# Kernel optimization log

Measured on AMD Instinct MI355X. Metric: run time of the kernel, lower is better.

The kernel has to match this reference:

```python
import jax, jax.numpy as jnp
import numpy as np

N_NODES = 100000
N_EDGES = 1600000
IN_C, HID_C, OUT_C = 128, 128, 64


def setup_inputs() -> dict:
    key = jax.random.key(0)
    k1, k2, k3, k4 = jax.random.split(key, 4)
    x = jax.random.normal(k1, (N_NODES, IN_C), dtype=jnp.float32)
    edge_index = jax.random.randint(k2, (2, N_EDGES), 0, N_NODES, dtype=jnp.int32)
    # Glorot-style init scale for the linear weights (matches PyG GCNConv default)
    W1 = jax.random.normal(k3, (IN_C, HID_C), dtype=jnp.float32) * (1.0 / np.sqrt(IN_C))
    b1 = jnp.zeros((HID_C,), dtype=jnp.float32)
    W2 = jax.random.normal(k4, (HID_C, OUT_C), dtype=jnp.float32) * (1.0 / np.sqrt(HID_C))
    b2 = jnp.zeros((OUT_C,), dtype=jnp.float32)
    return {"x": x, "edge_index": edge_index, "W1": W1, "b1": b1, "W2": W2, "b2": b2}


def _gcn_norm(edge_index, num_nodes):
    """Add self-loops and compute symmetric normalization deg^-1/2[src]*deg^-1/2[dst]."""
    src, dst = edge_index[0], edge_index[1]
    loop = jnp.arange(num_nodes, dtype=src.dtype)
    src_f = jnp.concatenate([src, loop])
    dst_f = jnp.concatenate([dst, loop])
    ones = jnp.ones_like(dst_f, dtype=jnp.float32)
    deg = jax.ops.segment_sum(ones, dst_f, num_segments=num_nodes)  # in-degree incl. self-loop
    deg_inv_sqrt = jnp.where(deg > 0, jax.lax.rsqrt(deg), 0.0)
    norm = deg_inv_sqrt[src_f] * deg_inv_sqrt[dst_f]  # [E+N]
    return src_f, dst_f, norm


def _gcn_conv(x, W, b, src_f, dst_f, norm, num_nodes):
    h = x @ W                              # [N, C_out] linear transform first
    msg = h[src_f] * norm[:, None]         # gather + scale, [E+N, C_out]
    agg = jax.ops.segment_sum(msg, dst_f, num_segments=num_nodes)  # scatter-add
    return agg + b


def reference(x, edge_index, W1, b1, W2, b2):
    n = x.shape[0]
    src_f, dst_f, norm = _gcn_norm(edge_index, n)
    h = jax.nn.relu(_gcn_conv(x, W1, b1, src_f, dst_f, norm, n))
    out = _gcn_conv(h, W2, b2, src_f, dst_f, norm, n)
    return out
```

## Files before the change

kernel.cpp:

```cpp
#include <hip/hip_runtime.h>


constexpr int BLK = 256;
constexpr int PCAP = 2560;
constexpr int CHUNK = 2048;
constexpr int NBMAX = 800;


__global__ __launch_bounds__(256)
void count_kernel(const int* __restrict__ dst, unsigned short* __restrict__ cnt,
                  int e, int nbuck) {
    __shared__ int hist[NBMAX];
    const int t = threadIdx.x;
    const int base = blockIdx.x * CHUNK;
    const int cend = min(CHUNK, e - base);

    for (int i = t; i < nbuck; i += 256) hist[i] = 0;
    __syncthreads();
    for (int i = t; i < cend; i += 256) atomicAdd(&hist[dst[base + i] >> 7], 1);
    __syncthreads();
    unsigned short* o = cnt + (size_t)blockIdx.x * nbuck;
    for (int i = t; i < nbuck; i += 256) o[i] = (unsigned short)hist[i];
}


__global__ __launch_bounds__(256)
void scan_bins_kernel(unsigned short* __restrict__ cnt, int* __restrict__ totals,
                      int nbuck, int nblk) {
    __shared__ int wsum[256];
    const int j = blockIdx.x;
    const int t = threadIdx.x;
    const int b0 = t * 4;
    int v[4];
    int s = 0;
#pragma unroll
    for (int q = 0; q < 4; ++q) {
        const int B = b0 + q;
        v[q] = (B < nblk) ? (int)cnt[(size_t)B * nbuck + j] : 0;
        s += v[q];
    }
    wsum[t] = s;
    __syncthreads();
    for (int off = 1; off < 256; off <<= 1) {
        int u = (t >= off) ? wsum[t - off] : 0;
        __syncthreads();
        wsum[t] += u;
        __syncthreads();
    }
    int run = (t > 0) ? wsum[t - 1] : 0;
#pragma unroll
    for (int q = 0; q < 4; ++q) {
        const int B = b0 + q;
        if (B < nblk) {
            cnt[(size_t)B * nbuck + j] = (unsigned short)min(run, PCAP);
            run += v[q];
        }
    }
    if (t == 255) totals[j] = run;
}


__global__ __launch_bounds__(256)
void place_kernel(const int* __restrict__ src, const int* __restrict__ dst,
                  const unsigned short* __restrict__ cnt, unsigned* __restrict__ ebuf,
                  int e, int nbuck) {
    __shared__ unsigned stage[CHUNK];
    __shared__ unsigned short keys[CHUNK];
    __shared__ int hist[NBMAX];
    __shared__ int excl[NBMAX];
    __shared__ int gbase[NBMAX];
    __shared__ int wsum[256];

    const int t = threadIdx.x;
    const int base = blockIdx.x * CHUNK;
    const int cend = min(CHUNK, e - base);

    for (int i = t; i < nbuck; i += 256) hist[i] = 0;
    __syncthreads();

    int dreg[8];
#pragma unroll
    for (int q = 0; q < 8; ++q) {
        const int i = t + q * 256;
        dreg[q] = (i < cend) ? dst[base + i] : -1;
        if (i < cend) atomicAdd(&hist[dreg[q] >> 7], 1);
    }
    __syncthreads();

    const int b0 = t * 4;
    int s0 = 0, s1 = 0, s2 = 0, s3 = 0;
    if (b0 < nbuck)     s0 = hist[b0];
    if (b0 + 1 < nbuck) s1 = hist[b0 + 1];
    if (b0 + 2 < nbuck) s2 = hist[b0 + 2];
    if (b0 + 3 < nbuck) s3 = hist[b0 + 3];
    wsum[t] = s0 + s1 + s2 + s3;
    __syncthreads();
    for (int off = 1; off < 256; off <<= 1) {
        int u = (t >= off) ? wsum[t - off] : 0;
        __syncthreads();
        wsum[t] += u;
        __syncthreads();
    }
    int run = (t > 0) ? wsum[t - 1] : 0;
    if (b0 < nbuck)     { excl[b0]     = run; hist[b0]     = run; run += s0; }
    if (b0 + 1 < nbuck) { excl[b0 + 1] = run; hist[b0 + 1] = run; run += s1; }
    if (b0 + 2 < nbuck) { excl[b0 + 2] = run; hist[b0 + 2] = run; run += s2; }
    if (b0 + 3 < nbuck) { excl[b0 + 3] = run; hist[b0 + 3] = run; run += s3; }
    {
        const unsigned short* cb = cnt + (size_t)blockIdx.x * nbuck;
        for (int i = t; i < nbuck; i += 256) gbase[i] = (int)cb[i];
    }
    __syncthreads();

#pragma unroll
    for (int q = 0; q < 8; ++q) {
        const int i = t + q * 256;
        if (i < cend) {
            const int s = src[base + i], d = dreg[q];
            const int bb = d >> 7;
            const int p = atomicAdd(&hist[bb], 1);
            stage[p] = ((unsigned)s << 7) | (unsigned)(d & 127);
            keys[p] = (unsigned short)bb;
        }
    }
    __syncthreads();

    for (int i = t; i < cend; i += 256) {
        const int bb = keys[i];
        const int p = gbase[bb] + (i - excl[bb]);
        if (p < PCAP) ebuf[(size_t)bb * PCAP + p] = stage[i];
    }
}


__global__ __launch_bounds__(256)
void build_kernel(const unsigned* __restrict__ ebuf, const int* __restrict__ totals,
                  float* __restrict__ dis, int2* __restrict__ rp,
                  int* __restrict__ esrc, int n) {
    __shared__ int packed[PCAP];
    __shared__ unsigned short rank[PCAP];
    __shared__ int hist[128];
    __shared__ int excl[128];
    __shared__ int start[128];

    const int b = blockIdx.x, t = threadIdx.x;
    const int base = b << 7;
    const int nloc = min(128, n - base);
    const int tot = min(totals[b], PCAP);

    if (t < 128) hist[t] = 0;
    __syncthreads();

    const unsigned* eb = ebuf + (size_t)b * PCAP;
    for (int i = t; i < tot; i += 256) {
        int v = (int)eb[i];
        packed[i] = v;
        rank[i] = (unsigned short)atomicAdd(&hist[v & 127], 1);
    }
    __syncthreads();

    if (t < 128) excl[t] = hist[t];
    __syncthreads();
    for (int off = 1; off < 128; off <<= 1) {
        int v = (t >= off && t < 128) ? excl[t - off] : 0;
        __syncthreads();
        if (t < 128) excl[t] += v;
        __syncthreads();
    }

    if (t < 128) {
        int deg = hist[t];
        int st = excl[t] - deg;
        start[t] = st;
        if (t < nloc) {
            dis[base + t] = rsqrtf((float)(deg + 1));
            int gs = b * PCAP + st;
            rp[base + t] = make_int2(gs, gs + deg);
        }
    }
    __syncthreads();

    int* eo = esrc + b * PCAP;
    for (int i = t; i < tot; i += 256) {
        int v = packed[i];
        eo[start[v & 127] + rank[i]] = v >> 7;
    }
}


__device__ __forceinline__ unsigned short f2bf(float f) {
    unsigned u = __float_as_uint(f);
    u += 0x7fffu + ((u >> 16) & 1u);
    return (unsigned short)(u >> 16);
}
__device__ __forceinline__ float bflo(unsigned u) { return __uint_as_float(u << 16); }
__device__ __forceinline__ float bfhi(unsigned u) { return __uint_as_float(u & 0xffff0000u); }
__device__ __forceinline__ unsigned pk2(short a, short b) {
    return (unsigned)(unsigned short)a | ((unsigned)(unsigned short)b << 16);
}

__device__ __forceinline__ void split2(float v, short& hi, short& lo) {
    unsigned short h = f2bf(v);
    float hf = __uint_as_float(((unsigned)h) << 16);
    hi = (short)h;
    lo = (short)f2bf(v - hf);
}

typedef __attribute__((ext_vector_type(8))) short bf16x8;
typedef __attribute__((ext_vector_type(4))) float f32x4;
#define MFMA_B16(a, b, c) __builtin_amdgcn_mfma_f32_16x16x32_bf16(a, b, c, 0, 0, 0)

__device__ __forceinline__ void split8(const float4& a, const float4& b, bf16x8& h, bf16x8& l) {
    short hh, ll;
    split2(a.x, hh, ll); h[0] = hh; l[0] = ll;
    split2(a.y, hh, ll); h[1] = hh; l[1] = ll;
    split2(a.z, hh, ll); h[2] = hh; l[2] = ll;
    split2(a.w, hh, ll); h[3] = hh; l[3] = ll;
    split2(b.x, hh, ll); h[4] = hh; l[4] = ll;
    split2(b.y, hh, ll); h[5] = hh; l[5] = ll;
    split2(b.z, hh, ll); h[6] = hh; l[6] = ll;
    split2(b.w, hh, ll); h[7] = hh; l[7] = ll;
}


__global__ void prep_b_kernel(const float* __restrict__ W1, const float* __restrict__ W2,
                              unsigned short* __restrict__ B1h, unsigned short* __restrict__ B1l,
                              unsigned short* __restrict__ B2h, unsigned short* __restrict__ B2l) {
    const int c = blockIdx.x;
    const int k = threadIdx.x;
    short h, l;
    if (c < 128) {
        split2(W1[(size_t)k * 128 + c], h, l);
        B1h[c * 128 + k] = (unsigned short)h;
        B1l[c * 128 + k] = (unsigned short)l;
    } else {
        const int c2 = c - 128;
        split2(W2[(size_t)k * 64 + c2], h, l);
        B2h[c2 * 128 + k] = (unsigned short)h;
        B2l[c2 * 128 + k] = (unsigned short)l;
    }
}


constexpr int BAS = 72;

__global__ __launch_bounds__(256, 4)
void gemm_mfma(const float* __restrict__ Af,
               const unsigned short* __restrict__ Bh, const unsigned short* __restrict__ Bl,
               const float* __restrict__ dis, unsigned* __restrict__ Cb, int nrows) {
    constexpr int COLS = 128;
    constexpr int CT = COLS / 16;
    constexpr int BE = COLS * BAS;
    constexpr int CSC = COLS + 8;
    constexpr int SMEM = (2 * BE * 2 > 128 * CSC * 2) ? 2 * BE * 2 : 128 * CSC * 2;

    __shared__ __align__(16) char smem[SMEM];
    short* sBh = (short*)smem;
    short* sBl = sBh + BE;

    const int t = threadIdx.x;
    const int rowbase = blockIdx.x * 128;
    const int wave = t >> 6;
    const int lane = t & 63;
    const int quad = lane >> 4;
    const int l16 = lane & 15;

    const int gr0 = rowbase + wave * 32 + l16;
    const int gr1 = gr0 + 16;

    f32x4 acc[2][CT];
#pragma unroll
    for (int rt = 0; rt < 2; ++rt)
#pragma unroll
        for (int ct = 0; ct < CT; ++ct) {
            f32x4 z = {0.f, 0.f, 0.f, 0.f};
            acc[rt][ct] = z;
        }

    for (int half = 0; half < 2; ++half) {
        {
            constexpr int NV = COLS * 8;
            uint4* dh = (uint4*)sBh;
            uint4* dl = (uint4*)sBl;
            const uint4* gh = (const uint4*)Bh;
            const uint4* gl = (const uint4*)Bl;
            for (int idx = t; idx < NV; idx += 256) {
                int c = idx >> 3, kq = idx & 7;
                int gidx = c * 16 + half * 8 + kq;
                int didx = c * 9 + kq;
                dh[didx] = gh[gidx];
                dl[didx] = gl[gidx];
            }
        }
        __syncthreads();

#pragma unroll
        for (int kc = 0; kc < 2; ++kc) {
            const int ko = kc * 32 + quad * 8;
            bf16x8 ah0, al0, ah1, al1;
            float4 va = {0.f, 0.f, 0.f, 0.f}, vb = va, vc = va, vd = va;
            if (gr0 < nrows) {
                const float4* ap = (const float4*)(Af + (size_t)gr0 * 128 + half * 64 + ko);
                va = ap[0]; vb = ap[1];
            }
            if (gr1 < nrows) {
                const float4* ap = (const float4*)(Af + (size_t)gr1 * 128 + half * 64 + ko);
                vc = ap[0]; vd = ap[1];
            }
            split8(va, vb, ah0, al0);
            split8(vc, vd, ah1, al1);
#pragma unroll
            for (int ct = 0; ct < CT; ++ct) {
                const int bo = (ct * 16 + l16) * BAS + ko;
                bf16x8 bh = *(const bf16x8*)&sBh[bo];
                bf16x8 bl = *(const bf16x8*)&sBl[bo];
                acc[0][ct] = MFMA_B16(ah0, bh, acc[0][ct]);
                acc[1][ct] = MFMA_B16(ah1, bh, acc[1][ct]);
                acc[0][ct] = MFMA_B16(al0, bh, acc[0][ct]);
                acc[1][ct] = MFMA_B16(al1, bh, acc[1][ct]);
                acc[0][ct] = MFMA_B16(ah0, bl, acc[0][ct]);
                acc[1][ct] = MFMA_B16(ah1, bl, acc[1][ct]);
            }
        }
        __syncthreads();
    }

    short* Cs = (short*)smem;
    float sv[2][4];
#pragma unroll
    for (int rt = 0; rt < 2; ++rt)
#pragma unroll
        for (int r = 0; r < 4; ++r) {
            int rr = rowbase + wave * 32 + rt * 16 + quad * 4 + r;
            sv[rt][r] = (rr < nrows) ? dis[rr] : 0.f;
        }
#pragma unroll
    for (int rt = 0; rt < 2; ++rt)
#pragma unroll
        for (int ct = 0; ct < CT; ++ct) {
            const int rb = wave * 32 + rt * 16 + quad * 4;
            const int c = ct * 16 + l16;
#pragma unroll
            for (int r = 0; r < 4; ++r)
                Cs[(rb + r) * CSC + c] = (short)f2bf(sv[rt][r] * acc[rt][ct][r]);
        }
    __syncthreads();

    {
        const int row = t >> 1, hf = t & 1;
        const int gr = rowbase + row;
        if (gr < nrows) {
            const uint4* cr = (const uint4*)&Cs[row * CSC + hf * (COLS / 2)];
            uint4* dstp = (uint4*)Cb + (size_t)gr * (COLS / 8) + hf * (COLS / 16);
#pragma unroll
            for (int i = 0; i < COLS / 16; ++i) dstp[i] = cr[i];
        }
    }
}


#define ACC8(v)                                           \
    acc[0] += bflo(v.x); acc[1] += bfhi(v.x);             \
    acc[2] += bflo(v.y); acc[3] += bfhi(v.y);             \
    acc[4] += bflo(v.z); acc[5] += bfhi(v.z);             \
    acc[6] += bflo(v.w); acc[7] += bfhi(v.w);

__global__ __launch_bounds__(512)
void gather_gemm_kernel(const int2* __restrict__ rp, const int* __restrict__ esrc,
                        const float* __restrict__ dis, const unsigned* __restrict__ hs,
                        const float* __restrict__ bias,
                        const unsigned short* __restrict__ B2h,
                        const unsigned short* __restrict__ B2l,
                        unsigned* __restrict__ h2b, int n) {
    constexpr int ASTR = 136;
    constexpr int CSTR = 72;
    __shared__ __align__(16) short sAh[32 * ASTR];
    __shared__ __align__(16) short sAl[32 * ASTR];

    const int t = threadIdx.x;
    const int base = blockIdx.x * 32;

    {
        const int nl = t >> 4;
        const int lc = t & 15;
        const int node = base + nl;

        if (node < n) {
            const uint4* h4 = (const uint4*)hs;
            const int2 se = rp[node];
            float acc[8];
            {
                uint4 v = h4[(size_t)node * 16 + lc];
                acc[0] = bflo(v.x); acc[1] = bfhi(v.x);
                acc[2] = bflo(v.y); acc[3] = bfhi(v.y);
                acc[4] = bflo(v.z); acc[5] = bfhi(v.z);
                acc[6] = bflo(v.w); acc[7] = bfhi(v.w);
            }
            int k = se.x;
            const int end = se.y;
            for (; k + 3 < end; k += 4) {
                int s0 = esrc[k], s1 = esrc[k + 1], s2 = esrc[k + 2], s3 = esrc[k + 3];
                uint4 v0 = h4[(size_t)s0 * 16 + lc];
                uint4 v1 = h4[(size_t)s1 * 16 + lc];
                uint4 v2 = h4[(size_t)s2 * 16 + lc];
                uint4 v3 = h4[(size_t)s3 * 16 + lc];
                ACC8(v0) ACC8(v1) ACC8(v2) ACC8(v3)
            }
            for (; k < end; ++k) {
                uint4 v = h4[(size_t)esrc[k] * 16 + lc];
                ACC8(v)
            }

            const float di = dis[node];
            const float4 ba = ((const float4*)bias)[lc * 2];
            const float4 bb = ((const float4*)bias)[lc * 2 + 1];
            float v0 = fmaxf(fmaf(di, acc[0], ba.x), 0.f);
            float v1 = fmaxf(fmaf(di, acc[1], ba.y), 0.f);
            float v2 = fmaxf(fmaf(di, acc[2], ba.z), 0.f);
            float v3 = fmaxf(fmaf(di, acc[3], ba.w), 0.f);
            float v4 = fmaxf(fmaf(di, acc[4], bb.x), 0.f);
            float v5 = fmaxf(fmaf(di, acc[5], bb.y), 0.f);
            float v6 = fmaxf(fmaf(di, acc[6], bb.z), 0.f);
            float v7 = fmaxf(fmaf(di, acc[7], bb.w), 0.f);

            short h0, l0, h1, l1, h2, l2, h3, l3, h4v, l4, h5, l5, h6, l6, h7, l7;
            split2(v0, h0, l0); split2(v1, h1, l1); split2(v2, h2, l2); split2(v3, h3, l3);
            split2(v4, h4v, l4); split2(v5, h5, l5); split2(v6, h6, l6); split2(v7, h7, l7);
            uint4 oh, ol;
            oh.x = pk2(h0, h1); oh.y = pk2(h2, h3); oh.z = pk2(h4v, h5); oh.w = pk2(h6, h7);
            ol.x = pk2(l0, l1); ol.y = pk2(l2, l3); ol.z = pk2(l4, l5);  ol.w = pk2(l6, l7);
            *(uint4*)&sAh[nl * ASTR + lc * 8] = oh;
            *(uint4*)&sAl[nl * ASTR + lc * 8] = ol;
        } else {
            uint4 z = {0u, 0u, 0u, 0u};
            *(uint4*)&sAh[nl * ASTR + lc * 8] = z;
            *(uint4*)&sAl[nl * ASTR + lc * 8] = z;
        }
    }
    __syncthreads();

    const int wave = t >> 6, lane = t & 63, quad = lane >> 4, l16 = lane & 15;
    const int rt = wave & 1;
    const int ct = wave >> 1;
    const int col = ct * 16 + l16;
    const int arow = (rt * 16 + l16) * ASTR;
    f32x4 c0 = {0.f, 0.f, 0.f, 0.f};
#pragma unroll
    for (int ks = 0; ks < 4; ++ks) {
        const int ko = ks * 32 + quad * 8;
        bf16x8 bh = *(const bf16x8*)&B2h[col * 128 + ko];
        bf16x8 bl = *(const bf16x8*)&B2l[col * 128 + ko];
        bf16x8 ah = *(const bf16x8*)&sAh[arow + ko];
        bf16x8 al = *(const bf16x8*)&sAl[arow + ko];
        c0 = MFMA_B16(ah, bh, c0);
        c0 = MFMA_B16(al, bh, c0);
        c0 = MFMA_B16(ah, bl, c0);
    }
    __syncthreads();

    short* Cs = sAh;
#pragma unroll
    for (int r = 0; r < 4; ++r) {
        const int row = rt * 16 + quad * 4 + r;
        const float d = (base + row < n) ? dis[base + row] : 0.f;
        Cs[row * CSTR + col] = (short)f2bf(d * c0[r]);
    }
    __syncthreads();
    if (t < 256) {
        const int row = t >> 3, l8 = t & 7;
        const int gr = base + row;
        if (gr < n)
            ((uint4*)h2b)[(size_t)gr * 8 + l8] = *(const uint4*)&Cs[row * CSTR + l8 * 8];
    }
}


#define ACCLO(v)                                          \
    acc[0] += bflo(v.x); acc[1] += bfhi(v.x);             \
    acc[2] += bflo(v.y); acc[3] += bfhi(v.y);             \
    acc[4] += bflo(v.z); acc[5] += bfhi(v.z);             \
    acc[6] += bflo(v.w); acc[7] += bfhi(v.w);
#define ACCHI(v)                                          \
    acc[8]  += bflo(v.x); acc[9]  += bfhi(v.x);           \
    acc[10] += bflo(v.y); acc[11] += bfhi(v.y);           \
    acc[12] += bflo(v.z); acc[13] += bfhi(v.z);           \
    acc[14] += bflo(v.w); acc[15] += bfhi(v.w);

__global__ __launch_bounds__(256)
void gather_out_kernel(const int2* __restrict__ rp, const int* __restrict__ esrc,
                       const float* __restrict__ dis, const unsigned* __restrict__ hs,
                       const float* __restrict__ bias, float* __restrict__ out, int n) {
    const int gid = blockIdx.x * BLK + threadIdx.x;
    const int node = gid >> 2;
    const int l4 = gid & 3;
    if (node >= n) return;

    const uint4* h4 = (const uint4*)hs;
    const int2 se = rp[node];

    float acc[16];
    {
        uint4 v0 = h4[(size_t)node * 8 + l4];
        uint4 v1 = h4[(size_t)node * 8 + 4 + l4];
        acc[0] = bflo(v0.x); acc[1] = bfhi(v0.x);
        acc[2] = bflo(v0.y); acc[3] = bfhi(v0.y);
        acc[4] = bflo(v0.z); acc[5] = bfhi(v0.z);
        acc[6] = bflo(v0.w); acc[7] = bfhi(v0.w);
        acc[8]  = bflo(v1.x); acc[9]  = bfhi(v1.x);
        acc[10] = bflo(v1.y); acc[11] = bfhi(v1.y);
        acc[12] = bflo(v1.z); acc[13] = bfhi(v1.z);
        acc[14] = bflo(v1.w); acc[15] = bfhi(v1.w);
    }

    int k = se.x;
    const int end = se.y;
    for (; k + 3 < end; k += 4) {
        int s0 = esrc[k], s1 = esrc[k + 1], s2 = esrc[k + 2], s3 = esrc[k + 3];
        uint4 a0 = h4[(size_t)s0 * 8 + l4], b0 = h4[(size_t)s0 * 8 + 4 + l4];
        uint4 a1 = h4[(size_t)s1 * 8 + l4], b1 = h4[(size_t)s1 * 8 + 4 + l4];
        uint4 a2 = h4[(size_t)s2 * 8 + l4], b2 = h4[(size_t)s2 * 8 + 4 + l4];
        uint4 a3 = h4[(size_t)s3 * 8 + l4], b3 = h4[(size_t)s3 * 8 + 4 + l4];
        ACCLO(a0) ACCHI(b0) ACCLO(a1) ACCHI(b1)
        ACCLO(a2) ACCHI(b2) ACCLO(a3) ACCHI(b3)
    }
    for (; k < end; ++k) {
        int s = esrc[k];
        uint4 a = h4[(size_t)s * 8 + l4], b = h4[(size_t)s * 8 + 4 + l4];
        ACCLO(a) ACCHI(b)
    }

    const float di = dis[node];
    const float4* b4 = (const float4*)bias;
    const float4 ba = b4[l4 * 2], bb = b4[l4 * 2 + 1];
    const float4 bc = b4[8 + l4 * 2], bd = b4[9 + l4 * 2];
    float4 o0, o1, o2, o3;
    o0.x = fmaf(di, acc[0],  ba.x); o0.y = fmaf(di, acc[1],  ba.y);
    o0.z = fmaf(di, acc[2],  ba.z); o0.w = fmaf(di, acc[3],  ba.w);
    o1.x = fmaf(di, acc[4],  bb.x); o1.y = fmaf(di, acc[5],  bb.y);
    o1.z = fmaf(di, acc[6],  bb.z); o1.w = fmaf(di, acc[7],  bb.w);
    o2.x = fmaf(di, acc[8],  bc.x); o2.y = fmaf(di, acc[9],  bc.y);
    o2.z = fmaf(di, acc[10], bc.z); o2.w = fmaf(di, acc[11], bc.w);
    o3.x = fmaf(di, acc[12], bd.x); o3.y = fmaf(di, acc[13], bd.y);
    o3.z = fmaf(di, acc[14], bd.z); o3.w = fmaf(di, acc[15], bd.w);
    float4* o4 = (float4*)out;
    o4[(size_t)node * 16 + l4 * 2]     = o0;
    o4[(size_t)node * 16 + l4 * 2 + 1] = o1;
    o4[(size_t)node * 16 + 8 + l4 * 2]     = o2;
    o4[(size_t)node * 16 + 8 + l4 * 2 + 1] = o3;
}

#undef ACC8
#undef ACCLO
#undef ACCHI


extern "C" void kernel_launch(void* const* d_in, const int* in_sizes, int n_in,
                              void* d_out, int out_size, void* d_ws, size_t ws_size,
                              hipStream_t stream) {
    const float* x  = (const float*)d_in[0];
    const int*   ei = (const int*)d_in[1];
    const float* W1 = (const float*)d_in[2];
    const float* b1 = (const float*)d_in[3];
    const float* W2 = (const float*)d_in[4];
    const float* b2 = (const float*)d_in[5];
    float* out = (float*)d_out;

    const int n = in_sizes[0] / 128;
    const int e = in_sizes[1] / 2;
    const int* src = ei;
    const int* dst = ei + e;

    char* ws = (char*)d_ws;
    float*    dis    = (float*)   (ws + 0x0);
    int2*     rp     = (int2*)    (ws + 0x80000);
    int*      totals = (int*)     (ws + 0x180000);
    unsigned short* B1h = (unsigned short*)(ws + 0x182000);
    unsigned short* B1l = (unsigned short*)(ws + 0x18A000);
    unsigned short* B2h = (unsigned short*)(ws + 0x192000);
    unsigned short* B2l = (unsigned short*)(ws + 0x196000);
    unsigned short* cnt = (unsigned short*)(ws + 0x1A0000);
    int*      esrc = (int*)     (ws + 0x2E0000);
    unsigned* hb   = (unsigned*)(ws + 0xB00000);
    unsigned* h2b  = (unsigned*)(ws + 0x2400000);
    unsigned* ebuf = (unsigned*)(ws + 0x2400000);

    const int nbuck = (n + 127) >> 7;
    const int nblk = (e + CHUNK - 1) / CHUNK;
    const int nb_g = (n + 127) / 128;

    prep_b_kernel<<<192, 128, 0, stream>>>(W1, W2, B1h, B1l, B2h, B2l);
    count_kernel<<<nblk, 256, 0, stream>>>(dst, cnt, e, nbuck);
    scan_bins_kernel<<<nbuck, 256, 0, stream>>>(cnt, totals, nbuck, nblk);
    place_kernel<<<nblk, 256, 0, stream>>>(src, dst, cnt, ebuf, e, nbuck);
    build_kernel<<<nbuck, 256, 0, stream>>>(ebuf, totals, dis, rp, esrc, n);

    gemm_mfma<<<nb_g, 256, 0, stream>>>(x, B1h, B1l, dis, hb, n);

    gather_gemm_kernel<<<(n + 31) / 32, 512, 0, stream>>>(
        rp, esrc, dis, hb, b1, B2h, B2l, h2b, n);

    gather_out_kernel<<<(n * 4 + BLK - 1) / BLK, BLK, 0, stream>>>(
        rp, esrc, dis, h2b, b2, out, n);
}
```

Before: 278.1 us.

## Sort per-node source lists in CSR build and remap layer-2 MFMA waves

The CSR build kernel now scatters edges into a shared-memory buffer, insertion-sorts each node's source indices, and writes the result out contiguously. Sorted sources should give later gathers better locality and allow coalesced global writes. Separately, the second-layer GEMM tail now has only the first four waves compute, each handling two 16-row tiles so the B fragments are reused. The sort adds a serial per-thread loop in the build kernel plus extra shared memory, and idles any waves beyond four in the GEMM.

Measured after the change: 305.1 us. 1.1x slower.

```diff
diff --git a/kernel.cpp b/kernel.cpp
--- a/kernel.cpp
+++ b/kernel.cpp
@@ -138,6 +138,7 @@
                   float* __restrict__ dis, int2* __restrict__ rp,
                   int* __restrict__ esrc, int n) {
     __shared__ int packed[PCAP];
+    __shared__ int sorted[PCAP];
     __shared__ unsigned short rank[PCAP];
     __shared__ int hist[128];
     __shared__ int excl[128];
@@ -180,11 +181,26 @@
     }
     __syncthreads();
 
-    int* eo = esrc + b * PCAP;
     for (int i = t; i < tot; i += 256) {
         int v = packed[i];
-        eo[start[v & 127] + rank[i]] = v >> 7;
-    }
+        sorted[start[v & 127] + rank[i]] = v >> 7;
+    }
+    __syncthreads();
+
+    if (t < 128) {
+        const int s0 = start[t];
+        const int e0 = s0 + hist[t];
+        for (int i = s0 + 1; i < e0; ++i) {
+            int v = sorted[i];
+            int j = i - 1;
+            while (j >= s0 && sorted[j] > v) { sorted[j + 1] = sorted[j]; --j; }
+            sorted[j + 1] = v;
+        }
+    }
+    __syncthreads();
+
+    int* eo = esrc + b * PCAP;
+    for (int i = t; i < tot; i += 256) eo[i] = sorted[i];
 }
 
 
@@ -440,30 +456,38 @@
     __syncthreads();
 
     const int wave = t >> 6, lane = t & 63, quad = lane >> 4, l16 = lane & 15;
-    const int rt = wave & 1;
-    const int ct = wave >> 1;
-    const int col = ct * 16 + l16;
-    const int arow = (rt * 16 + l16) * ASTR;
-    f32x4 c0 = {0.f, 0.f, 0.f, 0.f};
-#pragma unroll
-    for (int ks = 0; ks < 4; ++ks) {
-        const int ko = ks * 32 + quad * 8;
-        bf16x8 bh = *(const bf16x8*)&B2h[col * 128 + ko];
-        bf16x8 bl = *(const bf16x8*)&B2l[col * 128 + ko];
-        bf16x8 ah = *(const bf16x8*)&sAh[arow + ko];
-        bf16x8 al = *(const bf16x8*)&sAl[arow + ko];
-        c0 = MFMA_B16(ah, bh, c0);
-        c0 = MFMA_B16(al, bh, c0);
-        c0 = MFMA_B16(ah, bl, c0);
+    const int col = wave * 16 + l16;
+    f32x4 c0 = {0.f, 0.f, 0.f, 0.f}, c1 = c0;
+    if (t < 256) {
+#pragma unroll
+        for (int ks = 0; ks < 4; ++ks) {
+            const int ko = ks * 32 + quad * 8;
+            bf16x8 bh = *(const bf16x8*)&B2h[col * 128 + ko];
+            bf16x8 bl = *(const bf16x8*)&B2l[col * 128 + ko];
+            bf16x8 ah0 = *(const bf16x8*)&sAh[l16 * ASTR + ko];
+            bf16x8 al0 = *(const bf16x8*)&sAl[l16 * ASTR + ko];
+            bf16x8 ah1 = *(const bf16x8*)&sAh[(16 + l16) * ASTR + ko];
+            bf16x8 al1 = *(const bf16x8*)&sAl[(16 + l16) * ASTR + ko];
+            c0 = MFMA_B16(ah0, bh, c0);
+            c1 = MFMA_B16(ah1, bh, c1);
+            c0 = MFMA_B16(al0, bh, c0);
+            c1 = MFMA_B16(al1, bh, c1);
+            c0 = MFMA_B16(ah0, bl, c0);
+            c1 = MFMA_B16(ah1, bl, c1);
+        }
     }
     __syncthreads();
 
     short* Cs = sAh;
-#pragma unroll
-    for (int r = 0; r < 4; ++r) {
-        const int row = rt * 16 + quad * 4 + r;
-        const float d = (base + row < n) ? dis[base + row] : 0.f;
-        Cs[row * CSTR + col] = (short)f2bf(d * c0[r]);
+    if (t < 256) {
+#pragma unroll
+        for (int r = 0; r < 4; ++r) {
+            const int row0 = quad * 4 + r, row1 = 16 + quad * 4 + r;
+            const float d0 = (base + row0 < n) ? dis[base + row0] : 0.f;
+            const float d1 = (base + row1 < n) ? dis[base + row1] : 0.f;
+            Cs[row0 * CSTR + col] = (short)f2bf(d0 * c0[r]);
+            Cs[row1 * CSTR + col] = (short)f2bf(d1 * c1[r]);
+        }
     }
     __syncthreads();
     if (t < 256) {
```
